# Kernel optimization log

Hardware: AMD Instinct MI355X
Metric: run time of the kernel (lower is better)

Reference implementation:

```python
import jax, jax.numpy as jnp
import numpy as np

T, B, D, H = 512, 64, 256, 512


def setup_inputs() -> dict:
    key = jax.random.key(0)
    ks = jax.random.split(key, 6)
    scale = 1.0 / np.sqrt(D + H)
    return {
        "seqs": jax.random.normal(ks[0], (T, B, D), dtype=jnp.float32),
        "h": jnp.zeros((B, H), dtype=jnp.float32),
        "C": jnp.zeros((B, H), dtype=jnp.float32),
        "Wi": jax.random.normal(ks[1], (H, D + H), dtype=jnp.float32) * scale,
        "bi": jnp.zeros((H,), dtype=jnp.float32),
        "Wf": jax.random.normal(ks[2], (H, D + H), dtype=jnp.float32) * scale,
        "bf": jnp.zeros((H,), dtype=jnp.float32),
        "Wg": jax.random.normal(ks[3], (H, D + H), dtype=jnp.float32) * scale,
        "bg": jnp.zeros((H,), dtype=jnp.float32),
        "Wo": jax.random.normal(ks[4], (H, D + H), dtype=jnp.float32) * scale,
        "bo": jnp.zeros((H,), dtype=jnp.float32),
    }


def reference(seqs, h, C, Wi, bi, Wf, bf, Wg, bg, Wo, bo):
    # Fuse the 4 gate Linears into one matmul: W [4H, D+H], b [4H].
    W = jnp.concatenate([Wi, Wf, Wg, Wo], axis=0)
    b = jnp.concatenate([bi, bf, bg, bo], axis=0)

    def step(carry, x):
        h_t, c_t = carry
        merge = jnp.concatenate([h_t, x], axis=1)  # [B, H+D] (h first, as in torch code)
        gates = merge @ W.T + b                    # [B, 4H]
        i, f, g, o = jnp.split(gates, 4, axis=1)
        c_new = jax.nn.sigmoid(f) * c_t + jax.nn.sigmoid(i) * jnp.tanh(g)
        h_new = jax.nn.sigmoid(o) * jnp.tanh(c_new)
        return (h_new, c_new), h_new

    (_, cT), hs = jax.lax.scan(step, (h, C), seqs)
    allhidden = jnp.concatenate([h[None], hs], axis=0)  # [T+1, B, H], includes initial h
    return allhidden, cT
```

## Files before the change

### kernel.cpp

```cpp
#include <hip/hip_runtime.h>


#define TSTEPS 512
#define BATCH 64
#define DIN 256
#define HID 512
#define KTOT 768
#define BHID (BATCH * HID)
#define NB 8
#define NU 32
#define VROW 1064
#define POISON 0x7f7f7f7fu

typedef __attribute__((ext_vector_type(8))) short bf16x8;
typedef __attribute__((ext_vector_type(4))) float f32x4;

__device__ __forceinline__ float4 llc_load4(const float* p) {
    float4 r; asm volatile("global_load_dwordx4 %0, %1, off sc0 sc1" : "=&v"(r) : "v"(p)); return r;
}
__device__ __forceinline__ void llc_store1(float* p, float v) {
    asm volatile("global_store_dword %0, %1, off sc0 sc1" :: "v"(p), "v"(v) : "memory");
}
__device__ __forceinline__ unsigned short f2bf(float f) {
    unsigned u = __float_as_uint(f);
    return (unsigned short)((u + 0x7fffu + ((u >> 16) & 1u)) >> 16);
}

__global__ __launch_bounds__(512, 1)
void lstm_persistent(const float* __restrict__ seqs,
                     const float* __restrict__ h0,
                     const float* __restrict__ c0,
                     const float* __restrict__ Wi, const float* __restrict__ bi,
                     const float* __restrict__ Wf, const float* __restrict__ bff,
                     const float* __restrict__ Wg, const float* __restrict__ bg,
                     const float* __restrict__ Wo, const float* __restrict__ bo,
                     float* __restrict__ out)
{
    __shared__ __align__(16) short vv[NB * VROW];

    const int tid  = threadIdx.x;
    const int bid  = blockIdx.x;
    const int g    = bid >> 4;
    const int rblk = bid & 15;
    const int b0 = g * NB;
    const int u0 = rblk * NU;

    const int wv  = tid >> 6;
    const int l   = tid & 63;
    const int n16 = l & 15;
    const int khi = (l >> 4) & 3;
    const int bbr = l & 7;

    const int gsel = n16 & 3;
    const float* Wsel = (gsel == 0) ? Wi : (gsel == 1) ? Wf : (gsel == 2) ? Wg : Wo;
    const float* wrow = Wsel + (size_t)(u0 + 4 * wv + (n16 >> 2)) * KTOT;
    bf16x8 whi[24], wlo[24];
#pragma unroll
    for (int kt = 0; kt < 24; ++kt) {
        const int k0 = kt * 32 + khi * 8;
        const float4 a = *reinterpret_cast<const float4*>(wrow + k0);
        const float4 b = *reinterpret_cast<const float4*>(wrow + k0 + 4);
        const float vals[8] = {a.x, a.y, a.z, a.w, b.x, b.y, b.z, b.w};
        bf16x8 h8, l8;
#pragma unroll
        for (int i = 0; i < 8; ++i) {
            const unsigned short hv = f2bf(vals[i]);
            h8[i] = (short)hv;
            l8[i] = (short)f2bf(vals[i] - __uint_as_float((unsigned)hv << 16));
        }
        whi[kt] = h8; wlo[kt] = l8;
    }

    const int unit_d  = u0 + 4 * wv + khi;
    const int batch_d = b0 + (n16 & 7);
    const float bI = bi[unit_d],  bF = bff[unit_d];
    const float bG = bg[unit_d],  bO = bo[unit_d];
    float creg = c0[(size_t)batch_d * HID + unit_d];

    if (tid < 256) {
        const int uu = tid & 31, bb = tid >> 5;
        out[(size_t)(b0 + bb) * HID + u0 + uu] = h0[(size_t)(b0 + bb) * HID + u0 + uu];
    }

    {
        const int b = tid >> 6, k0 = (tid & 63) * 8;
        const float* hp = h0 + (size_t)(b0 + b) * HID + k0;
        const float4 t0 = reinterpret_cast<const float4*>(hp)[0];
        const float4 t1 = reinterpret_cast<const float4*>(hp)[1];
        const float hv[8] = {t0.x, t0.y, t0.z, t0.w, t1.x, t1.y, t1.z, t1.w};
        bf16x8 a8;
#pragma unroll
        for (int i = 0; i < 8; ++i) a8[i] = (short)f2bf(hv[i]);
        *reinterpret_cast<bf16x8*>(&vv[b * VROW + k0]) = a8;
    }
    if (tid < 256) {
        const int b = tid >> 5, kx = (tid & 31) * 8;
        const float* xp = seqs + (size_t)(b0 + b) * DIN + kx;
        const float4 t0 = reinterpret_cast<const float4*>(xp)[0];
        const float4 t1 = reinterpret_cast<const float4*>(xp)[1];
        const float xv[8] = {t0.x, t0.y, t0.z, t0.w, t1.x, t1.y, t1.z, t1.w};
        bf16x8 a8, la8;
#pragma unroll
        for (int i = 0; i < 8; ++i) {
            const unsigned short h1 = f2bf(xv[i]);
            a8[i]  = (short)h1;
            la8[i] = (short)f2bf(xv[i] - __uint_as_float((unsigned)h1 << 16));
        }
        *reinterpret_cast<bf16x8*>(&vv[b * VROW + 512 + kx]) = a8;
        *reinterpret_cast<bf16x8*>(&vv[b * VROW + 768 + kx]) = la8;
    }
    __syncthreads();

    const short* vrow = &vv[bbr * VROW + khi * 8];

    for (int t = 0; t < TSTEPS; ++t) {
        const int cb = tid >> 6, ck = (tid & 63) * 8;
        const float* hpf = out + (size_t)t * BHID + (size_t)(b0 + cb) * HID + ck;
        float4 hb0, hb1;
        if (t > 0) { hb0 = llc_load4(hpf); hb1 = llc_load4(hpf + 4); }

        f32x4 aA = {0.f,0.f,0.f,0.f}, aB = {0.f,0.f,0.f,0.f}, aC = {0.f,0.f,0.f,0.f};
#pragma unroll
        for (int kt = 0; kt < 8; ++kt) {
            const bf16x8 bh = *reinterpret_cast<const bf16x8*>(vrow + 512 + kt * 32);
            const bf16x8 bl = *reinterpret_cast<const bf16x8*>(vrow + 768 + kt * 32);
            aA = __builtin_amdgcn_mfma_f32_16x16x32_bf16(whi[16 + kt], bh, aA, 0, 0, 0);
            aB = __builtin_amdgcn_mfma_f32_16x16x32_bf16(wlo[16 + kt], bh, aB, 0, 0, 0);
            aC = __builtin_amdgcn_mfma_f32_16x16x32_bf16(whi[16 + kt], bl, aC, 0, 0, 0);
        }

        float4 xr0, xr1;
        const bool do_x = (t + 1 < TSTEPS) && (tid < 256);
        if (do_x) {
            const float* xp = seqs + (size_t)(t + 1) * BATCH * DIN
                            + (size_t)(b0 + (tid >> 5)) * DIN + (tid & 31) * 8;
            xr0 = reinterpret_cast<const float4*>(xp)[0];
            xr1 = reinterpret_cast<const float4*>(xp)[1];
        }

        if (t > 0) {
            unsigned miss = 0;
            for (;;) {
                asm volatile("s_waitcnt vmcnt(0)" ::: "memory");
                __builtin_amdgcn_sched_barrier(0);
                bool ok = true;
                ok &= (__float_as_uint(hb0.x) != POISON);
                ok &= (__float_as_uint(hb0.y) != POISON);
                ok &= (__float_as_uint(hb0.z) != POISON);
                ok &= (__float_as_uint(hb0.w) != POISON);
                ok &= (__float_as_uint(hb1.x) != POISON);
                ok &= (__float_as_uint(hb1.y) != POISON);
                ok &= (__float_as_uint(hb1.z) != POISON);
                ok &= (__float_as_uint(hb1.w) != POISON);
                if (ok) break;
                if (++miss > (1u << 20)) break;
                __builtin_amdgcn_s_sleep(1);
                hb0 = llc_load4(hpf); hb1 = llc_load4(hpf + 4);
            }
            const float hv[8] = {hb0.x, hb0.y, hb0.z, hb0.w, hb1.x, hb1.y, hb1.z, hb1.w};
            bf16x8 a8;
#pragma unroll
            for (int i = 0; i < 8; ++i) a8[i] = (short)f2bf(hv[i]);
            *reinterpret_cast<bf16x8*>(&vv[cb * VROW + ck]) = a8;
        }
        __syncthreads();

#pragma unroll
        for (int kt = 0; kt < 16; ++kt) {
            const bf16x8 bh = *reinterpret_cast<const bf16x8*>(vrow + kt * 32);
            aA = __builtin_amdgcn_mfma_f32_16x16x32_bf16(whi[kt], bh, aA, 0, 0, 0);
            aB = __builtin_amdgcn_mfma_f32_16x16x32_bf16(wlo[kt], bh, aB, 0, 0, 0);
        }
        const f32x4 gA = aA + aB + aC;

        if (n16 < 8) {
            const float gi = gA[0] + bI;
            const float gf = gA[1] + bF;
            const float gG = gA[2] + bG;
            const float go = gA[3] + bO;
            const float i_ = 1.f / (1.f + __expf(-gi));
            const float f_ = 1.f / (1.f + __expf(-gf));
            const float o_ = 1.f / (1.f + __expf(-go));
            float eg = __expf(-2.f * fabsf(gG));
            float tg = (1.f - eg) / (1.f + eg);
            tg = (gG < 0.f) ? -tg : tg;
            creg = f_ * creg + i_ * tg;
            float ec = __expf(-2.f * fabsf(creg));
            float tc = (1.f - ec) / (1.f + ec);
            tc = (creg < 0.f) ? -tc : tc;
            const float hn = o_ * tc;
            llc_store1(out + (size_t)(t + 1) * BHID + (size_t)batch_d * HID + unit_d, hn);
            if (t == TSTEPS - 1)
                out[(size_t)(TSTEPS + 1) * BHID + (size_t)batch_d * HID + unit_d] = creg;
        }

        if (do_x) {
            const int b = tid >> 5, kx = (tid & 31) * 8;
            const float xv[8] = {xr0.x, xr0.y, xr0.z, xr0.w, xr1.x, xr1.y, xr1.z, xr1.w};
            bf16x8 a8, la8;
#pragma unroll
            for (int i = 0; i < 8; ++i) {
                const unsigned short h1 = f2bf(xv[i]);
                a8[i]  = (short)h1;
                la8[i] = (short)f2bf(xv[i] - __uint_as_float((unsigned)h1 << 16));
            }
            *reinterpret_cast<bf16x8*>(&vv[b * VROW + 512 + kx]) = a8;
            *reinterpret_cast<bf16x8*>(&vv[b * VROW + 768 + kx]) = la8;
        }
        __syncthreads();
    }
}

extern "C" void kernel_launch(void* const* d_in, const int* in_sizes, int n_in,
                              void* d_out, int out_size, void* d_ws, size_t ws_size,
                              hipStream_t stream) {
    const float* seqs = (const float*)d_in[0];
    const float* h0   = (const float*)d_in[1];
    const float* c0   = (const float*)d_in[2];
    const float* Wi   = (const float*)d_in[3];
    const float* bi   = (const float*)d_in[4];
    const float* Wf   = (const float*)d_in[5];
    const float* bf   = (const float*)d_in[6];
    const float* Wg   = (const float*)d_in[7];
    const float* bg   = (const float*)d_in[8];
    const float* Wo   = (const float*)d_in[9];
    const float* bo   = (const float*)d_in[10];
    float* out = (float*)d_out;

    hipMemsetAsync((char*)out + (size_t)BHID * 4, 0x7f,
                   (size_t)TSTEPS * BHID * 4, stream);

    hipLaunchKernelGGL(lstm_persistent, dim3(128), dim3(512), 0, stream,
                       seqs, h0, c0, Wi, bi, Wf, bf, Wg, bg, Wo, bo, out);
}
```

Before: 1.251 ms.

## Double-buffer LDS h/x tiles to drop the end-of-step barrier

Splits the single shared-memory staging buffer into ping-pong h and x buffers indexed by timestep parity. The x tile for step t+2 is now written into the current parity slot, so the second __syncthreads per timestep can be removed. This cuts one block-wide barrier per step from the serial recurrence. In exchange it doubles LDS use, and it depends on the single remaining barrier being enough to order reads and writes across parities.

New measurement: 2.000 ms. 1.6x slower.

```diff
diff --git a/kernel.cpp b/kernel.cpp
--- a/kernel.cpp
+++ b/kernel.cpp
@@ -9,8 +9,9 @@
 #define BHID (BATCH * HID)
 #define NB 8
 #define NU 32
-#define VROW 1064
 #define POISON 0x7f7f7f7fu
+#define HROW 520
+#define XROW 264
 
 typedef __attribute__((ext_vector_type(8))) short bf16x8;
 typedef __attribute__((ext_vector_type(4))) float f32x4;
@@ -36,7 +37,9 @@
                      const float* __restrict__ Wo, const float* __restrict__ bo,
                      float* __restrict__ out)
 {
-    __shared__ __align__(16) short vv[NB * VROW];
+    __shared__ __align__(16) short hb_s[2][NB][HROW];
+    __shared__ __align__(16) short xh_s[2][NB][XROW];
+    __shared__ __align__(16) short xl_s[2][NB][XROW];
 
     const int tid  = threadIdx.x;
     const int bid  = blockIdx.x;
@@ -91,48 +94,54 @@
         bf16x8 a8;
 #pragma unroll
         for (int i = 0; i < 8; ++i) a8[i] = (short)f2bf(hv[i]);
-        *reinterpret_cast<bf16x8*>(&vv[b * VROW + k0]) = a8;
+        *reinterpret_cast<bf16x8*>(&hb_s[0][b][k0]) = a8;
     }
     if (tid < 256) {
         const int b = tid >> 5, kx = (tid & 31) * 8;
-        const float* xp = seqs + (size_t)(b0 + b) * DIN + kx;
-        const float4 t0 = reinterpret_cast<const float4*>(xp)[0];
-        const float4 t1 = reinterpret_cast<const float4*>(xp)[1];
-        const float xv[8] = {t0.x, t0.y, t0.z, t0.w, t1.x, t1.y, t1.z, t1.w};
-        bf16x8 a8, la8;
-#pragma unroll
-        for (int i = 0; i < 8; ++i) {
-            const unsigned short h1 = f2bf(xv[i]);
-            a8[i]  = (short)h1;
-            la8[i] = (short)f2bf(xv[i] - __uint_as_float((unsigned)h1 << 16));
-        }
-        *reinterpret_cast<bf16x8*>(&vv[b * VROW + 512 + kx]) = a8;
-        *reinterpret_cast<bf16x8*>(&vv[b * VROW + 768 + kx]) = la8;
+#pragma unroll
+        for (int s = 0; s < 2; ++s) {
+            const float* xp = seqs + (size_t)s * BATCH * DIN
+                            + (size_t)(b0 + b) * DIN + kx;
+            const float4 t0 = reinterpret_cast<const float4*>(xp)[0];
+            const float4 t1 = reinterpret_cast<const float4*>(xp)[1];
+            const float xv[8] = {t0.x, t0.y, t0.z, t0.w, t1.x, t1.y, t1.z, t1.w};
+            bf16x8 a8, la8;
+#pragma unroll
+            for (int i = 0; i < 8; ++i) {
+                const unsigned short h1 = f2bf(xv[i]);
+                a8[i]  = (short)h1;
+                la8[i] = (short)f2bf(xv[i] - __uint_as_float((unsigned)h1 << 16));
+            }
+            *reinterpret_cast<bf16x8*>(&xh_s[s][b][kx]) = a8;
+            *reinterpret_cast<bf16x8*>(&xl_s[s][b][kx]) = la8;
+        }
     }
     __syncthreads();
 
-    const short* vrow = &vv[bbr * VROW + khi * 8];
-
     for (int t = 0; t < TSTEPS; ++t) {
+        const int p = t & 1;
+
         const int cb = tid >> 6, ck = (tid & 63) * 8;
         const float* hpf = out + (size_t)t * BHID + (size_t)(b0 + cb) * HID + ck;
         float4 hb0, hb1;
         if (t > 0) { hb0 = llc_load4(hpf); hb1 = llc_load4(hpf + 4); }
 
         f32x4 aA = {0.f,0.f,0.f,0.f}, aB = {0.f,0.f,0.f,0.f}, aC = {0.f,0.f,0.f,0.f};
+        const short* xrh = &xh_s[p][bbr][khi * 8];
+        const short* xrl = &xl_s[p][bbr][khi * 8];
 #pragma unroll
         for (int kt = 0; kt < 8; ++kt) {
-            const bf16x8 bh = *reinterpret_cast<const bf16x8*>(vrow + 512 + kt * 32);
-            const bf16x8 bl = *reinterpret_cast<const bf16x8*>(vrow + 768 + kt * 32);
+            const bf16x8 bh = *reinterpret_cast<const bf16x8*>(xrh + kt * 32);
+            const bf16x8 bl = *reinterpret_cast<const bf16x8*>(xrl + kt * 32);
             aA = __builtin_amdgcn_mfma_f32_16x16x32_bf16(whi[16 + kt], bh, aA, 0, 0, 0);
             aB = __builtin_amdgcn_mfma_f32_16x16x32_bf16(wlo[16 + kt], bh, aB, 0, 0, 0);
             aC = __builtin_amdgcn_mfma_f32_16x16x32_bf16(whi[16 + kt], bl, aC, 0, 0, 0);
         }
 
         float4 xr0, xr1;
-        const bool do_x = (t + 1 < TSTEPS) && (tid < 256);
+        const bool do_x = (t + 2 < TSTEPS) && (tid < 256);
         if (do_x) {
-            const float* xp = seqs + (size_t)(t + 1) * BATCH * DIN
+            const float* xp = seqs + (size_t)(t + 2) * BATCH * DIN
                             + (size_t)(b0 + (tid >> 5)) * DIN + (tid & 31) * 8;
             xr0 = reinterpret_cast<const float4*>(xp)[0];
             xr1 = reinterpret_cast<const float4*>(xp)[1];
@@ -161,13 +170,14 @@
             bf16x8 a8;
 #pragma unroll
             for (int i = 0; i < 8; ++i) a8[i] = (short)f2bf(hv[i]);
-            *reinterpret_cast<bf16x8*>(&vv[cb * VROW + ck]) = a8;
+            *reinterpret_cast<bf16x8*>(&hb_s[p][cb][ck]) = a8;
         }
         __syncthreads();
 
+        const short* hr = &hb_s[p][bbr][khi * 8];
 #pragma unroll
         for (int kt = 0; kt < 16; ++kt) {
-            const bf16x8 bh = *reinterpret_cast<const bf16x8*>(vrow + kt * 32);
+            const bf16x8 bh = *reinterpret_cast<const bf16x8*>(hr + kt * 32);
             aA = __builtin_amdgcn_mfma_f32_16x16x32_bf16(whi[kt], bh, aA, 0, 0, 0);
             aB = __builtin_amdgcn_mfma_f32_16x16x32_bf16(wlo[kt], bh, aB, 0, 0, 0);
         }
@@ -204,10 +214,9 @@
                 a8[i]  = (short)h1;
                 la8[i] = (short)f2bf(xv[i] - __uint_as_float((unsigned)h1 << 16));
             }
-            *reinterpret_cast<bf16x8*>(&vv[b * VROW + 512 + kx]) = a8;
-            *reinterpret_cast<bf16x8*>(&vv[b * VROW + 768 + kx]) = la8;
-        }
-        __syncthreads();
+            *reinterpret_cast<bf16x8*>(&xh_s[p][b][kx]) = a8;
+            *reinterpret_cast<bf16x8*>(&xl_s[p][b][kx]) = la8;
+        }
     }
 }
 
```
